# Kernel optimization log

Measured on AMD Instinct MI355X. Metric: run time of the kernel, lower is better.

## Reference

```python
import jax, jax.numpy as jnp
import numpy as np
from jax import lax

K = 3        # KBA kernel size
GC = 4       # channels per group numerator (gc in torch code): g = c // GC
EPS = 1e-6   # LayerNorm2d eps


def conv2d(x, w, b=None, pad=0, groups=1):
    out = lax.conv_general_dilated(x, w, (1, 1), [(pad, pad), (pad, pad)],
                                   dimension_numbers=('NCHW', 'OIHW', 'NCHW'),
                                   feature_group_count=groups)
    return out if b is None else out + b[None, :, None, None]


def layernorm2d(x, w, b):
    mu = jnp.mean(x, axis=1, keepdims=True)
    var = jnp.mean((x - mu) ** 2, axis=1, keepdims=True)
    y = (x - mu) / jnp.sqrt(var + EPS)
    return w[None, :, None, None] * y + b[None, :, None, None]


def kba_fn(x, att, selfb, selfw):
    # x: (B,c,H,W) features; att: (B,nset,H,W) mixing coeffs
    B, c, H, W = x.shape
    nset = att.shape[1]
    g = c // GC; cg = GC; KK = K * K
    a = att.reshape(B, nset, H * W).transpose(0, 2, 1)              # (B,HW,nset)
    bias = a @ selfb[0]                                             # (B,HW,c)
    attk = (a @ selfw[0]).reshape(B, H * W, g, cg, cg * KK)         # per-pixel kernels
    pad = K // 2
    xp = jnp.pad(x, ((0, 0), (0, 0), (pad, pad), (pad, pad)))
    # im2col / unfold, channel-major then kernel position (matches torch unfold)
    patches = jnp.stack([xp[:, :, i:i + H, j:j + W] for i in range(K) for j in range(K)], axis=2)  # (B,c,KK,H,W)
    uf = patches.reshape(B, g, cg * KK, H * W).transpose(0, 3, 1, 2)  # (B,HW,g,cg*KK)
    out = jnp.einsum('bpgij,bpgj->bpgi', attk, uf).reshape(B, H * W, c) + bias
    return out.transpose(0, 2, 1).reshape(B, c, H, W)


def petformer(x, n1w, n1b, n2w, n2b,
              kdw1, kdw2, kc1a, kc1b, kproj,
              c2a_w, c2a_b, c2b_w, c2b_b, c211_w, c211_b,
              kw, kb, attgamma, ga1,
              temp, qkv_w, qkv_dw_w, mproj_w,
              ca1_w, ca1_b, ca2_w, ca2_b):
    B, C, H, W = x.shape
    # channel attention: global avg pool + 1x1 conv
    gap = jnp.mean(x, axis=(2, 3), keepdims=True)
    ca1 = conv2d(gap, ca1_w, ca1_b)
    ca2 = conv2d(gap, ca2_w, ca2_b)

    # ---- KBA branch ----
    xn = layernorm2d(x, n1w, n1b)
    hid = kdw1.shape[0]
    x1 = conv2d(conv2d(xn, kdw1), kdw2, pad=1, groups=hid)          # dwconv path
    interc = c2a_w.shape[0]
    a = conv2d(xn, c2a_w, c2a_b, pad=1, groups=interc)              # grouped 3x3
    a1, a2 = jnp.split(a, 2, axis=1)                                # SimpleGate
    a = conv2d(a1 * a2, c2b_w, c2b_b)                               # 1x1 -> nset
    att = a * attgamma + conv2d(xn, c211_w, c211_b)
    uf = conv2d(conv2d(xn, kc1a), kc1b, pad=1, groups=hid)          # conv1 path
    x2 = kba_fn(uf, att, kb, kw) * ga1 + uf
    kba_out = conv2d(jax.nn.gelu(x1, approximate=False) * x2, kproj)

    # ---- MDTA branch (transposed channel attention) ----
    xm = layernorm2d(x, n2w, n2b)
    qkv = conv2d(conv2d(xm, qkv_w), qkv_dw_w, pad=1, groups=3 * C)
    q, k, v = jnp.split(qkv, 3, axis=1)
    heads = temp.shape[0]
    _h = lambda t: t.reshape(B, heads, C // heads, H * W)
    q, k, v = _h(q), _h(k), _h(v)
    q = q / jnp.maximum(jnp.linalg.norm(q, axis=-1, keepdims=True), 1e-12)
    k = k / jnp.maximum(jnp.linalg.norm(k, axis=-1, keepdims=True), 1e-12)
    attn = jax.nn.softmax(jnp.einsum('bhcp,bhdp->bhcd', q, k) * temp, axis=-1)
    out = jnp.einsum('bhcd,bhdp->bhcp', attn, v).reshape(B, C, H, W)
    mdta_out = conv2d(out, mproj_w)

    return x + kba_out * ca1 + mdta_out * ca2


def setup_inputs() -> dict:
    key = jax.random.key(0)
    ks = iter(jax.random.split(key, 40))
    nrm = lambda shape, s=0.1: (jax.random.normal(next(ks), shape) * s).astype(jnp.float32)
    B, C, H, W = 4, 48, 64, 64
    HID, NSET, HEADS, INTERC = 96, 32, 8, 24
    return {
        'x': jax.random.normal(next(ks), (B, C, H, W), jnp.float32),
        'n1w': jnp.ones((C,), jnp.float32), 'n1b': jnp.zeros((C,), jnp.float32),
        'n2w': jnp.ones((C,), jnp.float32), 'n2b': jnp.zeros((C,), jnp.float32),
        'kdw1': nrm((HID, C, 1, 1)), 'kdw2': nrm((HID, 1, 3, 3)),
        'kc1a': nrm((HID, C, 1, 1)), 'kc1b': nrm((HID, 1, 3, 3)),
        'kproj': nrm((C, HID, 1, 1)),
        'c2a_w': nrm((INTERC, C // INTERC, 3, 3)), 'c2a_b': jnp.zeros((INTERC,), jnp.float32),
        'c2b_w': nrm((NSET, INTERC // 2, 1, 1)), 'c2b_b': jnp.zeros((NSET,), jnp.float32),
        'c211_w': nrm((NSET, C, 1, 1)), 'c211_b': jnp.zeros((NSET,), jnp.float32),
        'kw': nrm((1, NSET, HID * GC * K * K), 0.02), 'kb': nrm((1, NSET, HID), 0.02),
        'attgamma': jnp.full((1, NSET, 1, 1), 0.01, jnp.float32),
        'ga1': jnp.full((1, HID, 1, 1), 0.01, jnp.float32),
        'temp': jnp.ones((HEADS, 1, 1), jnp.float32),
        'qkv_w': nrm((3 * C, C, 1, 1)), 'qkv_dw_w': nrm((3 * C, 1, 3, 3)),
        'mproj_w': nrm((C, C, 1, 1)),
        'ca1_w': nrm((C, C, 1, 1)), 'ca1_b': jnp.zeros((C,), jnp.float32),
        'ca2_w': nrm((C, C, 1, 1)), 'ca2_b': jnp.zeros((C,), jnp.float32),
    }


def reference(x, n1w, n1b, n2w, n2b,
              kdw1, kdw2, kc1a, kc1b, kproj,
              c2a_w, c2a_b, c2b_w, c2b_b, c211_w, c211_b,
              kw, kb, attgamma, ga1,
              temp, qkv_w, qkv_dw_w, mproj_w,
              ca1_w, ca1_b, ca2_w, ca2_b):
    return petformer(x, n1w, n1b, n2w, n2b, kdw1, kdw2, kc1a, kc1b, kproj,
                     c2a_w, c2a_b, c2b_w, c2b_b, c211_w, c211_b,
                     kw, kb, attgamma, ga1, temp, qkv_w, qkv_dw_w, mproj_w,
                     ca1_w, ca1_b, ca2_w, ca2_b)
```

## Files before the change

### kernel.cpp

```cpp
#include <hip/hip_runtime.h>
#include <hip/hip_bf16.h>
#include <cstdint>

typedef unsigned short ushortT;
typedef __attribute__((ext_vector_type(8))) short short8;
typedef __attribute__((ext_vector_type(4))) float f32x4;
typedef __attribute__((ext_vector_type(4))) unsigned short ushort4v;

static constexpr int Bn = 4, Cc = 48, Hh = 64, Wd = 64, HW = 4096;
static constexpr int HID = 96, NSET = 32, INTERC = 24, HEADS = 8, CPH = 6;

static constexpr int FXN   = 0;
static constexpr int FA    = 786432;
static constexpr int FB    = 2359296;
static constexpr int FC    = 3932160;
static constexpr int FD    = 5505024;
static constexpr int FARAW = 7077888;
static constexpr int FATT  = 7471104;
static constexpr int FGAP  = 8781824;
static constexpr int FSP   = 8782400;
static constexpr int FW    = 8790000;
static constexpr int FATTB = 8937200;
static constexpr int FWT   = 9199344;
static constexpr int FXNB  = 9260784;
static constexpr int FXMB  = 9785072;
static constexpr int FHBF  = 10309360;
static constexpr int FWPW  = 11095792;
static constexpr int FWQK  = 11102960;
static constexpr int FWKP  = 11107568;
static constexpr int FWMP  = 11109872;
static constexpr int FQKVR = 11111424;
static constexpr int FQKV  = 13470720;

static constexpr int W_N1W=0, W_N1B=48, W_N2W=96, W_N2B=144;
static constexpr int W_KDW1=192, W_KDW2=4800, W_KC1A=5664, W_KC1B=10272;
static constexpr int W_KPROJ=11136, W_C2AW=15744, W_C2AB=16176;
static constexpr int W_C2BW=16200, W_C2BB=16584, W_C211W=16616, W_C211B=18152;
static constexpr int W_KW=18184, W_KB=128776, W_ATTG=131848, W_GA1=131880;
static constexpr int W_TEMP=131976, W_QKVW=131984, W_QKVDW=138896, W_MPROJ=140192;
static constexpr int W_CA1W=142496, W_CA1B=144800, W_CA2W=144848, W_CA2B=147152;

__device__ __forceinline__ float b2f(ushortT u) {
    union { uint32_t i; float f; } v; v.i = ((uint32_t)u) << 16; return v.f;
}
__device__ __forceinline__ ushortT f2b(float f) {
    union { float f; uint32_t i; } v; v.f = f;
    uint32_t i = v.i;
    uint32_t lsb = (i >> 16) & 1u;
    i += 0x7fffu + lsb;
    return (ushortT)(i >> 16);
}
__device__ __forceinline__ int dtype_bf16(const uint32_t* n1w_raw) {
    return n1w_raw[0] == 0x3F803F80u;
}
__device__ __forceinline__ ushortT raw_bf(const void* p, int idx, int fl) {
    return fl ? ((const ushortT*)p)[idx] : f2b(((const float*)p)[idx]);
}
__device__ __forceinline__ float raw_f(const void* p, int idx, int fl) {
    return fl ? b2f(((const ushortT*)p)[idx]) : ((const float*)p)[idx];
}

struct ConvPack {
    const void* src[27];
    int dstoff[27];
    int n[27];
};
struct RawW {
    const void* kdw1; const void* kc1a; const void* c211w; const void* qkvw;
    const void* kproj; const void* mproj; const void* kw; const void* kb;
    const void* n1w; const void* n1b; const void* n2w; const void* n2b;
};

__global__ void __launch_bounds__(256) k_prep(ConvPack p, RawW rw, float* __restrict__ dst,
                       ushortT* __restrict__ Wt, ushortT* __restrict__ Wpw,
                       ushortT* __restrict__ Wqk, ushortT* __restrict__ Wkp,
                       ushortT* __restrict__ Wmp,
                       const void* __restrict__ x, float* __restrict__ gap,
                       ushortT* __restrict__ xn, ushortT* __restrict__ xnb,
                       ushortT* __restrict__ xmb,
                       const uint32_t* __restrict__ n1w_raw) {
    int fl = dtype_bf16(n1w_raw);
    int y = blockIdx.y;
    if (y < 27) {
        int n = p.n[y];
        for (int i = blockIdx.x * 256 + threadIdx.x; i < n; i += 64 * 256) {
            dst[p.dstoff[y] + i] = raw_f(p.src[y], i, fl);
        }
    } else if (y == 27) {
        for (int u = blockIdx.x * 256 + threadIdx.x; u < 24 * 160 * 32; u += 64 * 256) {
            int n = u & 31;
            int rest = u >> 5;
            int r = rest % 160;
            int gr = rest / 160;
            ushortT out;
            if (r < 144) {
                int j = r >> 2, i = r & 3;
                out = raw_bf(rw.kw, n * 3456 + gr * 144 + i * 36 + j, fl);
            } else if (r < 148) {
                out = raw_bf(rw.kb, n * HID + gr * 4 + (r - 144), fl);
            } else out = 0;
            Wt[u] = out;
        }
    } else if (y == 28) {
        for (int u = blockIdx.x * 256 + threadIdx.x; u < 224 * 64; u += 64 * 256) {
            int co = u >> 6, c = u & 63;
            ushortT v = 0;
            if (c < 48) {
                if (co < 96)       v = raw_bf(rw.kdw1,  co * 48 + c, fl);
                else if (co < 192) v = raw_bf(rw.kc1a,  (co - 96) * 48 + c, fl);
                else               v = raw_bf(rw.c211w, (co - 192) * 48 + c, fl);
            }
            Wpw[u] = v;
        }
    } else if (y == 29) {
        for (int u = blockIdx.x * 256 + threadIdx.x; u < 144 * 64; u += 64 * 256) {
            int co = u >> 6, c = u & 63;
            Wqk[u] = (c < 48) ? raw_bf(rw.qkvw, co * 48 + c, fl) : (ushortT)0;
        }
    } else if (y == 30) {
        for (int u = blockIdx.x * 256 + threadIdx.x; u < 48 * 96; u += 64 * 256) {
            int co = u / 96, c = u % 96;
            Wkp[u] = raw_bf(rw.kproj, co * 96 + c, fl);
        }
    } else if (y == 31) {
        for (int u = blockIdx.x * 256 + threadIdx.x; u < 48 * 64; u += 64 * 256) {
            int co = u >> 6, c = u & 63;
            Wmp[u] = (c < 48) ? raw_bf(rw.mproj, co * 48 + c, fl) : (ushortT)0;
        }
    } else if (y == 32) {
        __shared__ float red[4];
        for (int bc = blockIdx.x; bc < Bn * Cc; bc += 64) {
            float s = 0.f;
            if (fl) {
                const ushortT* xb = (const ushortT*)x + bc * HW;
                for (int i = threadIdx.x; i < HW; i += 256) s += b2f(xb[i]);
            } else {
                const float* xb = (const float*)x + bc * HW;
                for (int i = threadIdx.x; i < HW; i += 256) s += xb[i];
            }
            #pragma unroll
            for (int o = 32; o > 0; o >>= 1) s += __shfl_down(s, o);
            int lane = threadIdx.x & 63, wv = threadIdx.x >> 6;
            if (lane == 0) red[wv] = s;
            __syncthreads();
            if (threadIdx.x == 0)
                gap[bc] = (red[0] + red[1] + red[2] + red[3]) * (1.f / HW);
            __syncthreads();
        }
    } else {
        int slice = y - 33;
        int tid = threadIdx.x;
        int pp = slice * 4096 + blockIdx.x * 64 + (tid >> 2);
        int part = tid & 3;
        int b = pp >> 12, hw = pp & 4095;
        const ushortT* xbh = (const ushortT*)x + (size_t)b * Cc * HW + hw;
        const float*  xbf = (const float*)x + (size_t)b * Cc * HW + hw;
        float v[12];
        float s = 0.f, ss = 0.f;
        #pragma unroll
        for (int j = 0; j < 12; j++) {
            int c = part * 12 + j;
            float t = fl ? b2f(xbh[c * HW]) : xbf[c * HW];
            v[j] = t; s += t; ss += t * t;
        }
        s  += __shfl_xor(s, 1);  s  += __shfl_xor(s, 2);
        ss += __shfl_xor(ss, 1); ss += __shfl_xor(ss, 2);
        float mu = s * (1.f / Cc);
        float var = ss * (1.f / Cc) - mu * mu;
        float r = rsqrtf(var + 1e-6f);
        uint32_t wn[6], wm[6];
        #pragma unroll
        for (int j2 = 0; j2 < 6; j2++) {
            int c0 = part * 12 + j2 * 2;
            float y0 = (v[j2 * 2] - mu) * r, y1 = (v[j2 * 2 + 1] - mu) * r;
            float n0 = raw_f(rw.n1w, c0, fl) * y0 + raw_f(rw.n1b, c0, fl);
            float n1 = raw_f(rw.n1w, c0 + 1, fl) * y1 + raw_f(rw.n1b, c0 + 1, fl);
            float m0 = raw_f(rw.n2w, c0, fl) * y0 + raw_f(rw.n2b, c0, fl);
            float m1 = raw_f(rw.n2w, c0 + 1, fl) * y1 + raw_f(rw.n2b, c0 + 1, fl);
            ushortT hn0 = f2b(n0), hn1 = f2b(n1);
            xn[(size_t)(b * Cc + c0) * HW + hw] = hn0;
            xn[(size_t)(b * Cc + c0 + 1) * HW + hw] = hn1;
            wn[j2] = (uint32_t)hn0 | ((uint32_t)hn1 << 16);
            wm[j2] = (uint32_t)f2b(m0) | ((uint32_t)f2b(m1) << 16);
        }
        uint32_t* dn = (uint32_t*)(xnb + (size_t)pp * 64 + part * 12);
        uint32_t* dm = (uint32_t*)(xmb + (size_t)pp * 64 + part * 12);
        #pragma unroll
        for (int j2 = 0; j2 < 6; j2++) { dn[j2] = wn[j2]; dm[j2] = wm[j2]; }
        if (part == 3) {
            uint4 zz; zz.x = 0; zz.y = 0; zz.z = 0; zz.w = 0;
            *(uint4*)(xnb + (size_t)pp * 64 + 48) = zz;
            *(uint4*)(xmb + (size_t)pp * 64 + 48) = zz;
        }
    }
}

__device__ __forceinline__ void row4_bf(const ushortT* row, int w0,
                                        float& lf, float& m0, float& m1,
                                        float& m2, float& m3, float& rt) {
    ushort4v mm = *(const ushort4v*)row;
    m0 = b2f(mm[0]); m1 = b2f(mm[1]); m2 = b2f(mm[2]); m3 = b2f(mm[3]);
    lf = (w0 > 0)  ? b2f(row[-1]) : 0.f;
    rt = (w0 < 60) ? b2f(row[4])  : 0.f;
}

__device__ __forceinline__ void dwconv8(const ushortT* plane, const float* wk,
                                        int h, int w0, float* aa) {
    #pragma unroll
    for (int ki = 0; ki < 3; ki++) {
        int hh = h + ki - 1;
        if ((unsigned)hh < 64u) {
            const ushortT* row = plane + hh * 64 + w0;
            ushort4v v0 = *(const ushort4v*)row;
            ushort4v v1 = *(const ushort4v*)(row + 4);
            float f[10];
            f[0] = (w0 > 0)  ? b2f(row[-1]) : 0.f;
            f[1] = b2f(v0[0]); f[2] = b2f(v0[1]); f[3] = b2f(v0[2]); f[4] = b2f(v0[3]);
            f[5] = b2f(v1[0]); f[6] = b2f(v1[1]); f[7] = b2f(v1[2]); f[8] = b2f(v1[3]);
            f[9] = (w0 < 56) ? b2f(row[8])  : 0.f;
            float k0 = wk[ki * 3], k1 = wk[ki * 3 + 1], k2 = wk[ki * 3 + 2];
            #pragma unroll
            for (int i = 0; i < 8; i++)
                aa[i] += k0 * f[i] + k1 * f[i + 1] + k2 * f[i + 2];
        }
    }
}

__global__ void __launch_bounds__(256) k_pw1m(const ushortT* __restrict__ xnb, const ushortT* __restrict__ xmb,
                       const ushortT* __restrict__ Wpw, const ushortT* __restrict__ Wqk,
                       const ushortT* __restrict__ xn, const float* __restrict__ wts,
                       ushortT* __restrict__ t1, ushortT* __restrict__ t2,
                       ushortT* __restrict__ attn_t, ushortT* __restrict__ qkvr,
                       ushortT* __restrict__ araw) {
    if (blockIdx.x >= 256) {
        if (blockIdx.y != 0) return;
        int sub = blockIdx.x - 256;
        int o = sub >> 4;
        int xb = sub & 15;
        int pbase = xb * 1024 + threadIdx.x * 4;
        int b = pbase >> 12, hw = pbase & 4095, h = hw >> 6, w0 = hw & 63;
        float bias = wts[W_C2AB + o];
        float a0 = bias, a1 = bias, a2 = bias, a3 = bias;
        #pragma unroll
        for (int ic = 0; ic < 2; ic++) {
            const ushortT* plane = xn + (size_t)(b * Cc + 2 * o + ic) * HW;
            const float* wk = wts + W_C2AW + (o * 2 + ic) * 9;
            #pragma unroll
            for (int ki = 0; ki < 3; ki++) {
                int hh = h + ki - 1;
                if ((unsigned)hh < 64u) {
                    const ushortT* row = plane + hh * 64 + w0;
                    float lf, m0, m1, m2, m3, rt;
                    row4_bf(row, w0, lf, m0, m1, m2, m3, rt);
                    float k0 = wk[ki * 3], k1 = wk[ki * 3 + 1], k2 = wk[ki * 3 + 2];
                    a0 += k0 * lf + k1 * m0 + k2 * m1;
                    a1 += k0 * m0 + k1 * m1 + k2 * m2;
                    a2 += k0 * m1 + k1 * m2 + k2 * m3;
                    a3 += k0 * m2 + k1 * m3 + k2 * rt;
                }
            }
        }
        ushort4v out;
        out[0] = f2b(a0); out[1] = f2b(a1); out[2] = f2b(a2); out[3] = f2b(a3);
        *(ushort4v*)(araw + (size_t)(b * INTERC + o) * HW + hw) = out;
        return;
    }
    int wave = threadIdx.x >> 6, lane = threadIdx.x & 63;
    int m = lane & 15, q = lane >> 4;
    int p = blockIdx.x * 64 + wave * 16 + m;
    int b = p >> 12, hw = p & 4095;
    if (blockIdx.y == 0) {
        short8 B0 = *(const short8*)(xnb + (size_t)p * 64 + q * 8);
        short8 B1 = *(const short8*)(xnb + (size_t)p * 64 + 32 + q * 8);
        #pragma unroll
        for (int t = 0; t < 14; t++) {
            short8 A0 = *(const short8*)(Wpw + (16 * t + m) * 64 + q * 8);
            short8 A1 = *(const short8*)(Wpw + (16 * t + m) * 64 + 32 + q * 8);
            f32x4 z = {0.f, 0.f, 0.f, 0.f};
            f32x4 D = __builtin_amdgcn_mfma_f32_16x16x32_bf16(A0, B0, z, 0, 0, 0);
            D = __builtin_amdgcn_mfma_f32_16x16x32_bf16(A1, B1, D, 0, 0, 0);
            #pragma unroll
            for (int g = 0; g < 4; g++) {
                int co = 16 * t + 4 * q + g;
                if (t < 6) t1[(size_t)(b * HID + co) * HW + hw] = f2b(D[g]);
                else if (t < 12) t2[(size_t)(b * HID + (co - 96)) * HW + hw] = f2b(D[g]);
                else {
                    int n = co - 192;
                    attn_t[(size_t)p * 32 + n] = f2b(D[g] + wts[W_C211B + n]);
                }
            }
        }
    } else {
        short8 C0 = *(const short8*)(xmb + (size_t)p * 64 + q * 8);
        short8 C1 = *(const short8*)(xmb + (size_t)p * 64 + 32 + q * 8);
        #pragma unroll
        for (int t = 0; t < 9; t++) {
            short8 A0 = *(const short8*)(Wqk + (16 * t + m) * 64 + q * 8);
            short8 A1 = *(const short8*)(Wqk + (16 * t + m) * 64 + 32 + q * 8);
            f32x4 z = {0.f, 0.f, 0.f, 0.f};
            f32x4 D = __builtin_amdgcn_mfma_f32_16x16x32_bf16(A0, C0, z, 0, 0, 0);
            D = __builtin_amdgcn_mfma_f32_16x16x32_bf16(A1, C1, D, 0, 0, 0);
            #pragma unroll
            for (int g = 0; g < 4; g++) {
                int co = 16 * t + 4 * q + g;
                qkvr[(size_t)(b * 144 + co) * HW + hw] = f2b(D[g]);
            }
        }
    }
}

__global__ void __launch_bounds__(256) k_dw(const ushortT* __restrict__ t1, const ushortT* __restrict__ t2,
                     const ushortT* __restrict__ qkvr, const ushortT* __restrict__ araw,
                     const ushortT* __restrict__ attn_t, const float* __restrict__ wts,
                     ushortT* __restrict__ x1g, ushortT* __restrict__ uf,
                     ushortT* __restrict__ qkv, ushortT* __restrict__ att_bf) {
    int y = blockIdx.y;

    if (y < 336) {
        int pbase = blockIdx.x * 2048 + threadIdx.x * 8;
        int b = pbase >> 12, hw = pbase & 4095, h = hw >> 6, w0 = hw & 63;
        const ushortT* plane;
        const float* wk;
        ushortT* dst;
        size_t idx;
        if (y < 96) {
            plane = t1 + (size_t)(b * HID + y) * HW;
            wk = wts + W_KDW2 + y * 9;
            dst = x1g; idx = (size_t)(b * HID + y) * HW + hw;
        } else if (y < 192) {
            int c = y - 96;
            plane = t2 + (size_t)(b * HID + c) * HW;
            wk = wts + W_KC1B + c * 9;
            dst = uf; idx = (size_t)(b * HID + c) * HW + hw;
        } else {
            int ch = y - 192;
            plane = qkvr + (size_t)(b * 144 + ch) * HW;
            wk = wts + W_QKVDW + ch * 9;
            dst = qkv; idx = (size_t)(b * 144 + ch) * HW + hw;
        }

        float aa[8];
        #pragma unroll
        for (int i = 0; i < 8; i++) aa[i] = 0.f;
        dwconv8(plane, wk, h, w0, aa);

        uint32_t pk[4];
        if (y < 96) {
            #pragma unroll
            for (int i = 0; i < 4; i++) {
                float g0 = 0.5f * aa[2*i]   * (1.f + erff(aa[2*i]   * 0.70710678118654752f));
                float g1 = 0.5f * aa[2*i+1] * (1.f + erff(aa[2*i+1] * 0.70710678118654752f));
                pk[i] = (uint32_t)f2b(g0) | ((uint32_t)f2b(g1) << 16);
            }
        } else {
            #pragma unroll
            for (int i = 0; i < 4; i++)
                pk[i] = (uint32_t)f2b(aa[2*i]) | ((uint32_t)f2b(aa[2*i+1]) << 16);
        }
        uint4 o; o.x = pk[0]; o.y = pk[1]; o.z = pk[2]; o.w = pk[3];
        *(uint4*)(dst + idx) = o;
    } else {
        int p = ((y - 336) * 8 + blockIdx.x) * 256 + threadIdx.x;
        int b = p >> 12, hw = p & 4095;
        const ushortT* ab = araw + (size_t)b * INTERC * HW + hw;
        float sg[12];
        #pragma unroll
        for (int i = 0; i < 12; i++) sg[i] = b2f(ab[i * HW]) * b2f(ab[(12 + i) * HW]);
        const ushortT* ct = attn_t + (size_t)p * 32;
        uint32_t packed[16];
        #pragma unroll
        for (int nq = 0; nq < 16; nq++) {
            float v2[2];
            #pragma unroll
            for (int u = 0; u < 2; u++) {
                int n = nq * 2 + u;
                float a = wts[W_C2BB + n];
                #pragma unroll
                for (int c = 0; c < 12; c++) a += wts[W_C2BW + n * 12 + c] * sg[c];
                v2[u] = wts[W_ATTG + n] * a + b2f(ct[n]);
            }
            packed[nq] = (uint32_t)f2b(v2[0]) | ((uint32_t)f2b(v2[1]) << 16);
        }
        uint4* dst = (uint4*)(att_bf + (size_t)p * 32);
        #pragma unroll
        for (int qd = 0; qd < 4; qd++) {
            uint4 v; v.x = packed[qd*4]; v.y = packed[qd*4+1]; v.z = packed[qd*4+2]; v.w = packed[qd*4+3];
            dst[qd] = v;
        }
    }
}

__global__ void __launch_bounds__(256) k_kba(const ushortT* __restrict__ att_bf, const ushortT* __restrict__ uf,
                     const ushortT* __restrict__ x1g, const ushortT* __restrict__ Wt,
                     const ushortT* __restrict__ qkv, const float* __restrict__ wts,
                     ushortT* __restrict__ h_bf, float* __restrict__ Sp) {
    __shared__ float red[48 * 4];
    __shared__ ushortT ufS[4][6][72];
    if (blockIdx.y == 24) {
        int sub = blockIdx.x;
        int bh = sub >> 1, chunk = sub & 1;
        int b = bh / HEADS, hd = bh % HEADS;
        const ushortT* qb = qkv + (size_t)(b * 144 + hd * CPH) * HW;
        const ushortT* kb = qkv + (size_t)(b * 144 + 48 + hd * CPH) * HW;
        float acc[48];
        #pragma unroll
        for (int t = 0; t < 48; t++) acc[t] = 0.f;
        #pragma unroll
        for (int i = 0; i < 8; i++) {
            int px = chunk * 2048 + i * 256 + threadIdx.x;
            float qv[CPH], kv[CPH];
            #pragma unroll
            for (int c = 0; c < CPH; c++) { qv[c] = b2f(qb[c * HW + px]); kv[c] = b2f(kb[c * HW + px]); }
            #pragma unroll
            for (int c = 0; c < CPH; c++) {
                #pragma unroll
                for (int d = 0; d < CPH; d++) acc[c * CPH + d] += qv[c] * kv[d];
                acc[36 + c] += qv[c] * qv[c];
                acc[42 + c] += kv[c] * kv[c];
            }
        }
        int lane = threadIdx.x & 63, wv = threadIdx.x >> 6;
        #pragma unroll
        for (int t = 0; t < 48; t++) {
            float v = acc[t];
            #pragma unroll
            for (int o = 32; o > 0; o >>= 1) v += __shfl_down(v, o);
            if (lane == 0) red[t * 4 + wv] = v;
        }
        __syncthreads();
        if (threadIdx.x < 48)
            Sp[(bh * 2 + chunk) * 48 + threadIdx.x] =
                red[threadIdx.x * 4] + red[threadIdx.x * 4 + 1] +
                red[threadIdx.x * 4 + 2] + red[threadIdx.x * 4 + 3];
        return;
    }

    int wave = threadIdx.x >> 6, lane = threadIdx.x & 63;
    int m = lane & 15, q = lane >> 4;
    int gr = blockIdx.y;
    int b = blockIdx.x >> 4;
    int h0 = (blockIdx.x & 15) * 4;

    #pragma unroll
    for (int pr = 0; pr < 24; pr += 4) {
        int pp = pr + wave;
        int ci = pp / 6, r = pp % 6;
        int hh = h0 - 1 + r;
        ushortT v = 0;
        if ((unsigned)hh < 64u)
            v = uf[(size_t)(b * HID + gr * 4 + ci) * HW + hh * 64 + lane];
        ufS[ci][r][lane + 1] = v;
        if (lane < 2) ufS[ci][r][lane * 65] = 0;
    }

    short8 A[10];
    const ushortT* wtg = Wt + gr * 160 * 32;
    #pragma unroll
    for (int t = 0; t < 10; t++)
        A[t] = *(const short8*)(wtg + (16 * t + m) * 32 + q * 8);

    __syncthreads();

    for (int tile = 0; tile < 4; tile++) {
        int p = blockIdx.x * 256 + wave * 64 + tile * 16 + m;
        int hw = p & 4095, w = hw & 63;

        short8 Bf = *(const short8*)(att_bf + (size_t)p * 32 + q * 8);

        f32x4 D[10];
        #pragma unroll
        for (int t = 0; t < 10; t++) {
            f32x4 z = {0.f, 0.f, 0.f, 0.f};
            D[t] = __builtin_amdgcn_mfma_f32_16x16x32_bf16(A[t], Bf, z, 0, 0, 0);
        }

        float s0 = 0.f, s1 = 0.f, s2 = 0.f, s3 = 0.f;
        #pragma unroll
        for (int t = 0; t < 9; t++) {
            int j = 4 * t + q;
            int ci = j / 9;
            int kk = j - 9 * ci;
            int ki = kk / 3, kj = kk - 3 * ki;
            float tap = b2f(ufS[ci][wave + ki][w + kj]);
            s0 += D[t][0] * tap;
            s1 += D[t][1] * tap;
            s2 += D[t][2] * tap;
            s3 += D[t][3] * tap;
        }
        s0 += D[9][0]; s1 += D[9][1]; s2 += D[9][2]; s3 += D[9][3];

        s0 += __shfl_xor(s0, 16); s0 += __shfl_xor(s0, 32);
        s1 += __shfl_xor(s1, 16); s1 += __shfl_xor(s1, 32);
        s2 += __shfl_xor(s2, 16); s2 += __shfl_xor(s2, 32);
        s3 += __shfl_xor(s3, 16); s3 += __shfl_xor(s3, 32);

        float sel = (q == 0) ? s0 : ((q == 1) ? s1 : ((q == 2) ? s2 : s3));
        int ch = gr * 4 + q;
        size_t idx = (size_t)(b * HID + ch) * HW + hw;
        float x2 = sel * wts[W_GA1 + ch] + b2f(ufS[q][wave + 1][w + 1]);
        float hv = b2f(x1g[idx]) * x2;
        h_bf[(size_t)p * 96 + ch] = f2b(hv);
    }
}

__global__ void __launch_bounds__(256) k_finalm(const void* __restrict__ x, const uint32_t* __restrict__ n1w_raw,
                        const ushortT* __restrict__ h_bf, const ushortT* __restrict__ Wkp,
                        const ushortT* __restrict__ Wmp, const ushortT* __restrict__ qkv,
                        const float* __restrict__ Sp, const float* __restrict__ gap,
                        const float* __restrict__ wts, void* __restrict__ out) {
    int fl = dtype_bf16(n1w_raw);
    int wave = threadIdx.x >> 6, lane = threadIdx.x & 63;
    int m = lane & 15, q = lane >> 4;
    int p = blockIdx.x * 64 + wave * 16 + m;
    int hw = p & 4095;
    int wl = wave * 16 + m;
    int bblk = (blockIdx.x * 64) >> 12;
    int hw0 = (blockIdx.x * 64) & 4095;

    __shared__ float sm[384];
    __shared__ float S_l[288];
    __shared__ float caL[96];
    __shared__ ushortT vS[48 * 68];

    for (int i2 = threadIdx.x; i2 < 48 * 64; i2 += 256) {
        int ch = i2 >> 6, w2 = i2 & 63;
        vS[ch * 68 + w2] = qkv[(size_t)(bblk * 144 + 96 + ch) * HW + hw0 + w2];
    }
    for (int i = threadIdx.x; i < 384; i += 256) {
        int hd = i / 48, k = i % 48;
        int bh = bblk * HEADS + hd;
        sm[i] = Sp[(bh * 2 + 0) * 48 + k] + Sp[(bh * 2 + 1) * 48 + k];
    }
    __syncthreads();
    if (threadIdx.x < 48) {
        int hd = threadIdx.x / 6, c = threadIdx.x % 6;
        const float* base = sm + hd * 48;
        float rqv = 1.f / fmaxf(sqrtf(base[36 + c]), 1e-12f);
        float tmp = wts[W_TEMP + hd];
        float row[CPH];
        #pragma unroll
        for (int d = 0; d < CPH; d++) {
            float rkv = 1.f / fmaxf(sqrtf(base[42 + d]), 1e-12f);
            row[d] = base[c * CPH + d] * rqv * rkv * tmp;
        }
        float mx = row[0];
        #pragma unroll
        for (int d = 1; d < CPH; d++) mx = fmaxf(mx, row[d]);
        float sum = 0.f;
        #pragma unroll
        for (int d = 0; d < CPH; d++) { row[d] = expf(row[d] - mx); sum += row[d]; }
        float inv = 1.f / sum;
        #pragma unroll
        for (int d = 0; d < CPH; d++) S_l[hd * 36 + c * CPH + d] = row[d] * inv;
    }
    if (threadIdx.x >= 64 && threadIdx.x < 160) {
        int i = threadIdx.x - 64;
        int which = i / 48, co = i % 48;
        const float* g = gap + bblk * Cc;
        float sacc = wts[(which ? W_CA2B : W_CA1B) + co];
        #pragma unroll
        for (int c = 0; c < Cc; c++)
            sacc += wts[(which ? W_CA2W : W_CA1W) + co * Cc + c] * g[c];
        caL[i] = sacc;
    }
    __syncthreads();

    short8 H0 = *(const short8*)(h_bf + (size_t)p * 96 + q * 8);
    short8 H1 = *(const short8*)(h_bf + (size_t)p * 96 + 32 + q * 8);
    short8 H2 = *(const short8*)(h_bf + (size_t)p * 96 + 64 + q * 8);
    f32x4 Dk[3];
    #pragma unroll
    for (int t = 0; t < 3; t++) {
        short8 A0 = *(const short8*)(Wkp + (16 * t + m) * 96 + q * 8);
        short8 A1 = *(const short8*)(Wkp + (16 * t + m) * 96 + 32 + q * 8);
        short8 A2 = *(const short8*)(Wkp + (16 * t + m) * 96 + 64 + q * 8);
        f32x4 z = {0.f, 0.f, 0.f, 0.f};
        f32x4 D = __builtin_amdgcn_mfma_f32_16x16x32_bf16(A0, H0, z, 0, 0, 0);
        D = __builtin_amdgcn_mfma_f32_16x16x32_bf16(A1, H1, D, 0, 0, 0);
        Dk[t] = __builtin_amdgcn_mfma_f32_16x16x32_bf16(A2, H2, D, 0, 0, 0);
    }

    short8 Bm0, Bm1;
    #pragma unroll
    for (int jj = 0; jj < 8; jj++) {
        int c0 = q * 8 + jj;
        int hd0 = c0 / 6, cc0 = c0 - 6 * hd0;
        float a = 0.f;
        #pragma unroll
        for (int d = 0; d < CPH; d++)
            a += S_l[hd0 * 36 + cc0 * 6 + d] * b2f(vS[(hd0 * 6 + d) * 68 + wl]);
        Bm0[jj] = (short)f2b(a);
        int c1 = 32 + q * 8 + jj;
        float bv = 0.f;
        if (c1 < 48) {
            int hd1 = c1 / 6, cc1 = c1 - 6 * hd1;
            #pragma unroll
            for (int d = 0; d < CPH; d++)
                bv += S_l[hd1 * 36 + cc1 * 6 + d] * b2f(vS[(hd1 * 6 + d) * 68 + wl]);
        }
        Bm1[jj] = (short)f2b(bv);
    }

    #pragma unroll
    for (int t = 0; t < 3; t++) {
        short8 A0 = *(const short8*)(Wmp + (16 * t + m) * 64 + q * 8);
        short8 A1 = *(const short8*)(Wmp + (16 * t + m) * 64 + 32 + q * 8);
        f32x4 z = {0.f, 0.f, 0.f, 0.f};
        f32x4 D = __builtin_amdgcn_mfma_f32_16x16x32_bf16(A0, Bm0, z, 0, 0, 0);
        D = __builtin_amdgcn_mfma_f32_16x16x32_bf16(A1, Bm1, D, 0, 0, 0);
        #pragma unroll
        for (int g = 0; g < 4; g++) {
            int co = 16 * t + 4 * q + g;
            int idx = (bblk * Cc + co) * HW + hw;
            float xv = fl ? b2f(((const ushortT*)x)[idx]) : ((const float*)x)[idx];
            float res = xv + Dk[t][g] * caL[co] + D[g] * caL[48 + co];
            if (fl) ((ushortT*)out)[idx] = f2b(res);
            else    ((float*)out)[idx] = res;
        }
    }
}

extern "C" void kernel_launch(void* const* d_in, const int* in_sizes, int n_in,
                              void* d_out, int out_size, void* d_ws, size_t ws_size,
                              hipStream_t stream) {
    float* ws_f = (float*)d_ws;

    ushortT* xn    = (ushortT*)(ws_f + FXN);
    ushortT* bufA  = (ushortT*)(ws_f + FA);
    ushortT* bufB  = (ushortT*)(ws_f + FB);
    ushortT* x1g   = (ushortT*)(ws_f + FC);
    ushortT* uf    = (ushortT*)(ws_f + FD);
    ushortT* araw  = (ushortT*)(ws_f + FARAW);
    ushortT* attn_t= (ushortT*)(ws_f + FATT);
    float* gap   = ws_f + FGAP;
    float* Sp    = ws_f + FSP;
    float* wts   = ws_f + FW;
    ushortT* att_bf  = (ushortT*)(ws_f + FATTB);
    ushortT* Wt      = (ushortT*)(ws_f + FWT);
    ushortT* xnb     = (ushortT*)(ws_f + FXNB);
    ushortT* xmb     = (ushortT*)(ws_f + FXMB);
    ushortT* h_bf    = (ushortT*)(ws_f + FHBF);
    ushortT* Wpw     = (ushortT*)(ws_f + FWPW);
    ushortT* Wqk     = (ushortT*)(ws_f + FWQK);
    ushortT* Wkp     = (ushortT*)(ws_f + FWKP);
    ushortT* Wmp     = (ushortT*)(ws_f + FWMP);
    ushortT* qkvr    = (ushortT*)(ws_f + FQKVR);
    ushortT* qkv     = (ushortT*)(ws_f + FQKV);

    const uint32_t* n1w_raw = (const uint32_t*)d_in[1];

    static const int wsizes[27] = {48,48,48,48,4608,864,4608,864,4608,432,24,384,32,
                                   1536,32,110592,3072,32,96,8,6912,1296,2304,2304,48,2304,48};
    static const int woffs[27] = {W_N1W,W_N1B,W_N2W,W_N2B,W_KDW1,W_KDW2,W_KC1A,W_KC1B,
                                  W_KPROJ,W_C2AW,W_C2AB,W_C2BW,W_C2BB,W_C211W,W_C211B,
                                  W_KW,W_KB,W_ATTG,W_GA1,W_TEMP,W_QKVW,W_QKVDW,W_MPROJ,
                                  W_CA1W,W_CA1B,W_CA2W,W_CA2B};
    ConvPack cp;
    for (int i = 0; i < 27; i++) {
        cp.src[i] = d_in[i + 1];
        cp.dstoff[i] = woffs[i];
        cp.n[i] = wsizes[i];
    }
    RawW rw;
    rw.kdw1 = d_in[5]; rw.kc1a = d_in[7]; rw.c211w = d_in[14]; rw.qkvw = d_in[21];
    rw.kproj = d_in[9]; rw.mproj = d_in[23]; rw.kw = d_in[16]; rw.kb = d_in[17];
    rw.n1w = d_in[1]; rw.n1b = d_in[2]; rw.n2w = d_in[3]; rw.n2b = d_in[4];

    k_prep<<<dim3(64, 37), 256, 0, stream>>>(cp, rw, wts, Wt, Wpw, Wqk, Wkp, Wmp,
                                             d_in[0], gap, xn, xnb, xmb, n1w_raw);
    k_pw1m<<<dim3(640, 2), 256, 0, stream>>>(xnb, xmb, Wpw, Wqk, xn, wts,
                                             bufA, bufB, attn_t, qkvr, araw);
    k_dw<<<dim3(8, 344), 256, 0, stream>>>(bufA, bufB, qkvr, araw, attn_t, wts,
                                           x1g, uf, qkv, att_bf);
    k_kba<<<dim3(64, 25), 256, 0, stream>>>(att_bf, uf, x1g, Wt, qkv, wts, h_bf, Sp);
    k_finalm<<<dim3(256), 256, 0, stream>>>(d_in[0], n1w_raw, h_bf, Wkp, Wmp,
                                            qkv, Sp, gap, wts, d_out);
}
```

Measured before the change: 186.1 us.

## Store only per-pixel LayerNorm stats and apply normalization inside consumer kernel

```diff
diff --git a/kernel.cpp b/kernel.cpp
--- a/kernel.cpp
+++ b/kernel.cpp
@@ -10,7 +10,6 @@
 static constexpr int Bn = 4, Cc = 48, Hh = 64, Wd = 64, HW = 4096;
 static constexpr int HID = 96, NSET = 32, INTERC = 24, HEADS = 8, CPH = 6;
 
-static constexpr int FXN   = 0;
 static constexpr int FA    = 786432;
 static constexpr int FB    = 2359296;
 static constexpr int FC    = 3932160;
@@ -22,8 +21,7 @@
 static constexpr int FW    = 8790000;
 static constexpr int FATTB = 8937200;
 static constexpr int FWT   = 9199344;
-static constexpr int FXNB  = 9260784;
-static constexpr int FXMB  = 9785072;
+static constexpr int FSTAT = 9260784;
 static constexpr int FHBF  = 10309360;
 static constexpr int FWPW  = 11095792;
 static constexpr int FWQK  = 11102960;
@@ -76,8 +74,7 @@
                        ushortT* __restrict__ Wqk, ushortT* __restrict__ Wkp,
                        ushortT* __restrict__ Wmp,
                        const void* __restrict__ x, float* __restrict__ gap,
-                       ushortT* __restrict__ xn, ushortT* __restrict__ xnb,
-                       ushortT* __restrict__ xmb,
+                       float2* __restrict__ stats,
                        const uint32_t* __restrict__ n1w_raw) {
     int fl = dtype_bf16(n1w_raw);
     int y = blockIdx.y;
@@ -155,53 +152,39 @@
         int b = pp >> 12, hw = pp & 4095;
         const ushortT* xbh = (const ushortT*)x + (size_t)b * Cc * HW + hw;
         const float*  xbf = (const float*)x + (size_t)b * Cc * HW + hw;
-        float v[12];
         float s = 0.f, ss = 0.f;
         #pragma unroll
         for (int j = 0; j < 12; j++) {
             int c = part * 12 + j;
             float t = fl ? b2f(xbh[c * HW]) : xbf[c * HW];
-            v[j] = t; s += t; ss += t * t;
+            s += t; ss += t * t;
         }
         s  += __shfl_xor(s, 1);  s  += __shfl_xor(s, 2);
         ss += __shfl_xor(ss, 1); ss += __shfl_xor(ss, 2);
         float mu = s * (1.f / Cc);
         float var = ss * (1.f / Cc) - mu * mu;
         float r = rsqrtf(var + 1e-6f);
-        uint32_t wn[6], wm[6];
-        #pragma unroll
-        for (int j2 = 0; j2 < 6; j2++) {
-            int c0 = part * 12 + j2 * 2;
-            float y0 = (v[j2 * 2] - mu) * r, y1 = (v[j2 * 2 + 1] - mu) * r;
-            float n0 = raw_f(rw.n1w, c0, fl) * y0 + raw_f(rw.n1b, c0, fl);
-            float n1 = raw_f(rw.n1w, c0 + 1, fl) * y1 + raw_f(rw.n1b, c0 + 1, fl);
-            float m0 = raw_f(rw.n2w, c0, fl) * y0 + raw_f(rw.n2b, c0, fl);
-            float m1 = raw_f(rw.n2w, c0 + 1, fl) * y1 + raw_f(rw.n2b, c0 + 1, fl);
-            ushortT hn0 = f2b(n0), hn1 = f2b(n1);
-            xn[(size_t)(b * Cc + c0) * HW + hw] = hn0;
-            xn[(size_t)(b * Cc + c0 + 1) * HW + hw] = hn1;
-            wn[j2] = (uint32_t)hn0 | ((uint32_t)hn1 << 16);
-            wm[j2] = (uint32_t)f2b(m0) | ((uint32_t)f2b(m1) << 16);
-        }
-        uint32_t* dn = (uint32_t*)(xnb + (size_t)pp * 64 + part * 12);
-        uint32_t* dm = (uint32_t*)(xmb + (size_t)pp * 64 + part * 12);
-        #pragma unroll
-        for (int j2 = 0; j2 < 6; j2++) { dn[j2] = wn[j2]; dm[j2] = wm[j2]; }
-        if (part == 3) {
-            uint4 zz; zz.x = 0; zz.y = 0; zz.z = 0; zz.w = 0;
-            *(uint4*)(xnb + (size_t)pp * 64 + 48) = zz;
-            *(uint4*)(xmb + (size_t)pp * 64 + 48) = zz;
-        }
-    }
-}
-
-__device__ __forceinline__ void row4_bf(const ushortT* row, int w0,
-                                        float& lf, float& m0, float& m1,
-                                        float& m2, float& m3, float& rt) {
-    ushort4v mm = *(const ushort4v*)row;
-    m0 = b2f(mm[0]); m1 = b2f(mm[1]); m2 = b2f(mm[2]); m3 = b2f(mm[3]);
-    lf = (w0 > 0)  ? b2f(row[-1]) : 0.f;
-    rt = (w0 < 60) ? b2f(row[4])  : 0.f;
+        if (part == 0) {
+            float2 o; o.x = mu; o.y = r;
+            stats[pp] = o;
+        }
+    }
+}
+
+__device__ __forceinline__ void load6(const void* plane, int fl, int base, int w0, float* f) {
+    if (fl) {
+        const ushortT* rp = (const ushortT*)plane + base;
+        ushort4v mm = *(const ushort4v*)rp;
+        f[1] = b2f(mm[0]); f[2] = b2f(mm[1]); f[3] = b2f(mm[2]); f[4] = b2f(mm[3]);
+        f[0] = (w0 > 0)  ? b2f(rp[-1]) : 0.f;
+        f[5] = (w0 < 60) ? b2f(rp[4])  : 0.f;
+    } else {
+        const float* rp = (const float*)plane + base;
+        float4 mm = *(const float4*)rp;
+        f[1] = mm.x; f[2] = mm.y; f[3] = mm.z; f[4] = mm.w;
+        f[0] = (w0 > 0)  ? rp[-1] : 0.f;
+        f[5] = (w0 < 60) ? rp[4]  : 0.f;
+    }
 }
 
 __device__ __forceinline__ void dwconv8(const ushortT* plane, const float* wk,
@@ -226,12 +209,14 @@
     }
 }
 
-__global__ void __launch_bounds__(256) k_pw1m(const ushortT* __restrict__ xnb, const ushortT* __restrict__ xmb,
+__global__ void __launch_bounds__(256) k_pw1m(const void* __restrict__ x, const float2* __restrict__ stats,
                        const ushortT* __restrict__ Wpw, const ushortT* __restrict__ Wqk,
-                       const ushortT* __restrict__ xn, const float* __restrict__ wts,
+                       RawW rw, const float* __restrict__ wts,
                        ushortT* __restrict__ t1, ushortT* __restrict__ t2,
                        ushortT* __restrict__ attn_t, ushortT* __restrict__ qkvr,
-                       ushortT* __restrict__ araw) {
+                       ushortT* __restrict__ araw,
+                       const uint32_t* __restrict__ n1w_raw) {
+    int fl = dtype_bf16(n1w_raw);
     if (blockIdx.x >= 256) {
         if (blockIdx.y != 0) return;
         int sub = blockIdx.x - 256;
@@ -239,25 +224,56 @@
         int xb = sub & 15;
         int pbase = xb * 1024 + threadIdx.x * 4;
         int b = pbase >> 12, hw = pbase & 4095, h = hw >> 6, w0 = hw & 63;
+        const float2* st = stats + b * 4096;
+        float nw0 = raw_f(rw.n1w, 2 * o, fl),     nb0 = raw_f(rw.n1b, 2 * o, fl);
+        float nw1 = raw_f(rw.n1w, 2 * o + 1, fl), nb1 = raw_f(rw.n1b, 2 * o + 1, fl);
+        const void* pl0;
+        const void* pl1;
+        if (fl) {
+            pl0 = (const void*)((const ushortT*)x + (size_t)(b * Cc + 2 * o) * HW);
+            pl1 = (const void*)((const ushortT*)x + (size_t)(b * Cc + 2 * o + 1) * HW);
+        } else {
+            pl0 = (const void*)((const float*)x + (size_t)(b * Cc + 2 * o) * HW);
+            pl1 = (const void*)((const float*)x + (size_t)(b * Cc + 2 * o + 1) * HW);
+        }
+        const float* wk = wts + W_C2AW + (o * 2) * 9;
         float bias = wts[W_C2AB + o];
         float a0 = bias, a1 = bias, a2 = bias, a3 = bias;
         #pragma unroll
-        for (int ic = 0; ic < 2; ic++) {
-            const ushortT* plane = xn + (size_t)(b * Cc + 2 * o + ic) * HW;
-            const float* wk = wts + W_C2AW + (o * 2 + ic) * 9;
-            #pragma unroll
-            for (int ki = 0; ki < 3; ki++) {
-                int hh = h + ki - 1;
-                if ((unsigned)hh < 64u) {
-                    const ushortT* row = plane + hh * 64 + w0;
-                    float lf, m0, m1, m2, m3, rt;
-                    row4_bf(row, w0, lf, m0, m1, m2, m3, rt);
-                    float k0 = wk[ki * 3], k1 = wk[ki * 3 + 1], k2 = wk[ki * 3 + 2];
-                    a0 += k0 * lf + k1 * m0 + k2 * m1;
-                    a1 += k0 * m0 + k1 * m1 + k2 * m2;
-                    a2 += k0 * m1 + k1 * m2 + k2 * m3;
-                    a3 += k0 * m2 + k1 * m3 + k2 * rt;
+        for (int ki = 0; ki < 3; ki++) {
+            int hh = h + ki - 1;
+            if ((unsigned)hh < 64u) {
+                int base = hh * 64 + w0;
+                float mu[6], rr[6];
+                #pragma unroll
+                for (int i = 0; i < 6; i++) {
+                    int c = w0 + i - 1;
+                    if ((unsigned)c < 64u) {
+                        float2 s2 = st[hh * 64 + c];
+                        mu[i] = s2.x; rr[i] = s2.y;
+                    } else { mu[i] = 0.f; rr[i] = 0.f; }
                 }
+                float f[6], g[6];
+                float k0a = wk[ki * 3], k1a = wk[ki * 3 + 1], k2a = wk[ki * 3 + 2];
+                float k0b = wk[9 + ki * 3], k1b = wk[9 + ki * 3 + 1], k2b = wk[9 + ki * 3 + 2];
+                load6(pl0, fl, base, w0, f);
+                g[0] = (w0 > 0)  ? nw0 * ((f[0] - mu[0]) * rr[0]) + nb0 : 0.f;
+                #pragma unroll
+                for (int i = 1; i < 5; i++) g[i] = nw0 * ((f[i] - mu[i]) * rr[i]) + nb0;
+                g[5] = (w0 < 60) ? nw0 * ((f[5] - mu[5]) * rr[5]) + nb0 : 0.f;
+                a0 += k0a * g[0] + k1a * g[1] + k2a * g[2];
+                a1 += k0a * g[1] + k1a * g[2] + k2a * g[3];
+                a2 += k0a * g[2] + k1a * g[3] + k2a * g[4];
+                a3 += k0a * g[3] + k1a * g[4] + k2a * g[5];
+                load6(pl1, fl, base, w0, f);
+                g[0] = (w0 > 0)  ? nw1 * ((f[0] - mu[0]) * rr[0]) + nb1 : 0.f;
+                #pragma unroll
+                for (int i = 1; i < 5; i++) g[i] = nw1 * ((f[i] - mu[i]) * rr[i]) + nb1;
+                g[5] = (w0 < 60) ? nw1 * ((f[5] - mu[5]) * rr[5]) + nb1 : 0.f;
+                a0 += k0b * g[0] + k1b * g[1] + k2b * g[2];
+                a1 += k0b * g[1] + k1b * g[2] + k2b * g[3];
+                a2 += k0b * g[2] + k1b * g[3] + k2b * g[4];
+                a3 += k0b * g[3] + k1b * g[4] + k2b * g[5];
             }
         }
         ushort4v out;
@@ -265,13 +281,37 @@
         *(ushort4v*)(araw + (size_t)(b * INTERC + o) * HW + hw) = out;
         return;
     }
+
+    __shared__ ushortT xS[64][72];
+    int blk = blockIdx.x;
+    int p0 = blk * 64;
+    int b = p0 >> 12, hw0 = p0 & 4095;
+    const float2* st = stats + b * 4096 + hw0;
+    const void* nwp = blockIdx.y ? rw.n2w : rw.n1w;
+    const void* nbp = blockIdx.y ? rw.n2b : rw.n1b;
+    const ushortT* xh = (const ushortT*)x + (size_t)b * Cc * HW + hw0;
+    const float*  xf = (const float*)x  + (size_t)b * Cc * HW + hw0;
+    for (int i = threadIdx.x; i < 48 * 64; i += 256) {
+        int ch = i >> 6, w = i & 63;
+        float v = fl ? b2f(xh[(size_t)ch * HW + w]) : xf[(size_t)ch * HW + w];
+        float2 s2 = st[w];
+        float yv = (v - s2.x) * s2.y;
+        xS[w][ch] = f2b(raw_f(nwp, ch, fl) * yv + raw_f(nbp, ch, fl));
+    }
+    for (int i = threadIdx.x; i < 16 * 64; i += 256) {
+        int ch = 48 + (i >> 6), w = i & 63;
+        xS[w][ch] = 0;
+    }
+    __syncthreads();
+
     int wave = threadIdx.x >> 6, lane = threadIdx.x & 63;
     int m = lane & 15, q = lane >> 4;
-    int p = blockIdx.x * 64 + wave * 16 + m;
-    int b = p >> 12, hw = p & 4095;
+    int pl = wave * 16 + m;
+    int p = p0 + pl;
+    int hw = p & 4095;
+    short8 B0 = *(const short8*)&xS[pl][q * 8];
+    short8 B1 = *(const short8*)&xS[pl][32 + q * 8];
     if (blockIdx.y == 0) {
-        short8 B0 = *(const short8*)(xnb + (size_t)p * 64 + q * 8);
-        short8 B1 = *(const short8*)(xnb + (size_t)p * 64 + 32 + q * 8);
         #pragma unroll
         for (int t = 0; t < 14; t++) {
             short8 A0 = *(const short8*)(Wpw + (16 * t + m) * 64 + q * 8);
@@ -291,15 +331,13 @@
             }
         }
     } else {
-        short8 C0 = *(const short8*)(xmb + (size_t)p * 64 + q * 8);
-        short8 C1 = *(const short8*)(xmb + (size_t)p * 64 + 32 + q * 8);
         #pragma unroll
         for (int t = 0; t < 9; t++) {
             short8 A0 = *(const short8*)(Wqk + (16 * t + m) * 64 + q * 8);
             short8 A1 = *(const short8*)(Wqk + (16 * t + m) * 64 + 32 + q * 8);
             f32x4 z = {0.f, 0.f, 0.f, 0.f};
-            f32x4 D = __builtin_amdgcn_mfma_f32_16x16x32_bf16(A0, C0, z, 0, 0, 0);
-            D = __builtin_amdgcn_mfma_f32_16x16x32_bf16(A1, C1, D, 0, 0, 0);
+            f32x4 D = __builtin_amdgcn_mfma_f32_16x16x32_bf16(A0, B0, z, 0, 0, 0);
+            D = __builtin_amdgcn_mfma_f32_16x16x32_bf16(A1, B1, D, 0, 0, 0);
             #pragma unroll
             for (int g = 0; g < 4; g++) {
                 int co = 16 * t + 4 * q + g;
@@ -625,7 +663,6 @@
                               hipStream_t stream) {
     float* ws_f = (float*)d_ws;
 
-    ushortT* xn    = (ushortT*)(ws_f + FXN);
     ushortT* bufA  = (ushortT*)(ws_f + FA);
     ushortT* bufB  = (ushortT*)(ws_f + FB);
     ushortT* x1g   = (ushortT*)(ws_f + FC);
@@ -637,8 +674,7 @@
     float* wts   = ws_f + FW;
     ushortT* att_bf  = (ushortT*)(ws_f + FATTB);
     ushortT* Wt      = (ushortT*)(ws_f + FWT);
-    ushortT* xnb     = (ushortT*)(ws_f + FXNB);
-    ushortT* xmb     = (ushortT*)(ws_f + FXMB);
+    float2* stats    = (float2*)(ws_f + FSTAT);
     ushortT* h_bf    = (ushortT*)(ws_f + FHBF);
     ushortT* Wpw     = (ushortT*)(ws_f + FWPW);
     ushortT* Wqk     = (ushortT*)(ws_f + FWQK);
@@ -667,9 +703,9 @@
     rw.n1w = d_in[1]; rw.n1b = d_in[2]; rw.n2w = d_in[3]; rw.n2b = d_in[4];
 
     k_prep<<<dim3(64, 37), 256, 0, stream>>>(cp, rw, wts, Wt, Wpw, Wqk, Wkp, Wmp,
-                                             d_in[0], gap, xn, xnb, xmb, n1w_raw);
-    k_pw1m<<<dim3(640, 2), 256, 0, stream>>>(xnb, xmb, Wpw, Wqk, xn, wts,
-                                             bufA, bufB, attn_t, qkvr, araw);
+                                             d_in[0], gap, stats, n1w_raw);
+    k_pw1m<<<dim3(640, 2), 256, 0, stream>>>(d_in[0], stats, Wpw, Wqk, rw, wts,
+                                             bufA, bufB, attn_t, qkvr, araw, n1w_raw);
     k_dw<<<dim3(8, 344), 256, 0, stream>>>(bufA, bufB, qkvr, araw, attn_t, wts,
                                            x1g, uf, qkv, att_bf);
     k_kba<<<dim3(64, 25), 256, 0, stream>>>(att_bf, uf, x1g, Wt, qkv, wts, h_bf, Sp);
```

New measurement: 187.6 us. No clear change (+0.8%).
